# Optimization experiments

Measured on AMD Instinct MI355X. Metric: run time of the kernel, lower is better.

Reference implementation:

```python
import jax, jax.numpy as jnp
import numpy as np

B, IN, H = 4096, 1024, 1024


def setup_inputs() -> dict:
    key = jax.random.key(0)
    ks = jax.random.split(key, 12)
    s = float(np.sqrt(6.0 / (IN + H)))  # xavier-uniform-like scale
    u = lambda k, shp: jax.random.uniform(k, shp, jnp.float32, -s, s)
    return {
        "x": jax.random.normal(ks[0], (B, IN), jnp.float32),
        "h_prev": jax.random.normal(ks[1], (B, H), jnp.float32),
        "c_prev": jax.random.normal(ks[2], (B, H), jnp.float32),
        "n_prev": jnp.ones((B, H), jnp.float32),
        "m_prev": jnp.zeros((B, H), jnp.float32),
        "Wi_x": u(ks[3], (H, IN)), "bi": jnp.zeros((H,), jnp.float32), "Wi_h": u(ks[4], (H, H)),
        "Wf_x": u(ks[5], (H, IN)), "bf": jnp.full((H,), 2.0, jnp.float32), "Wf_h": u(ks[6], (H, H)),
        "Wz_x": u(ks[7], (H, IN)), "bz": jnp.zeros((H,), jnp.float32), "Wz_h": u(ks[8], (H, H)),
        "Wo_x": u(ks[9], (H, IN)), "bo": jnp.zeros((H,), jnp.float32), "Wo_h": u(ks[10], (H, H)),
    }


def reference(x, h_prev, c_prev, n_prev, m_prev,
              Wi_x, bi, Wi_h, Wf_x, bf, Wf_h,
              Wz_x, bz, Wz_h, Wo_x, bo, Wo_h):
    # 8 projections (x-side with bias, h-side without), torch Linear: y = x @ W.T + b
    i_tilde = x @ Wi_x.T + bi + h_prev @ Wi_h.T
    f_aff   = x @ Wf_x.T + bf + h_prev @ Wf_h.T
    z_aff   = x @ Wz_x.T + bz + h_prev @ Wz_h.T
    o_aff   = x @ Wo_x.T + bo + h_prev @ Wo_h.T

    # forget_as_exp=False path: sigmoid forget gate, log-domain stabilizer
    log_f = jnp.log(jnp.clip(jax.nn.sigmoid(f_aff), 1e-8, None))
    m_t = jnp.maximum(log_f + m_prev, i_tilde)
    i_prime = jnp.exp(i_tilde - m_t)
    f_prime = jnp.exp(log_f + m_prev - m_t)

    z = jnp.tanh(z_aff)
    c_t = f_prime * c_prev + i_prime * z
    n_t = f_prime * n_prev + i_prime
    h_t = jax.nn.sigmoid(o_aff) * (c_t / jnp.clip(n_t, 1e-6, None))
    return h_t, c_t, n_t, m_t
```

## Files before the change

kernel.cpp:

```cpp
#include <hip/hip_runtime.h>
#include <stdint.h>


#define B_DIM 4096
#define K_DIM 2048

typedef __bf16 bf16x8 __attribute__((ext_vector_type(8)));
typedef float f32x4 __attribute__((ext_vector_type(4)));
typedef unsigned short ushort8 __attribute__((ext_vector_type(8)));

__device__ __forceinline__ unsigned short f2bf(float f) {
  unsigned u = __float_as_uint(f);
  u += 0x7fffu + ((u >> 16) & 1u);
  return (unsigned short)(u >> 16);
}
__device__ __forceinline__ float bf2f(unsigned short u) {
  return __uint_as_float(((unsigned)u) << 16);
}

__device__ __forceinline__ ushort8 load8_as_bf16(const void* base, size_t off, bool isbf) {
  if (isbf) return *(const ushort8*)((const unsigned short*)base + off);
  const float* f = (const float*)base + off;
  float4 v0 = ((const float4*)f)[0];
  float4 v1 = ((const float4*)f)[1];
  ushort8 o;
  o[0] = f2bf(v0.x); o[1] = f2bf(v0.y); o[2] = f2bf(v0.z); o[3] = f2bf(v0.w);
  o[4] = f2bf(v1.x); o[5] = f2bf(v1.y); o[6] = f2bf(v1.z); o[7] = f2bf(v1.w);
  return o;
}

__global__ void pack_all(const void* __restrict__ xv, const void* __restrict__ hv,
                         const void* __restrict__ Wix, const void* __restrict__ Wih,
                         const void* __restrict__ Wfx, const void* __restrict__ Wfh,
                         const void* __restrict__ Wzx, const void* __restrict__ Wzh,
                         const void* __restrict__ Wox, const void* __restrict__ Woh,
                         unsigned short* __restrict__ Apk, unsigned short* __restrict__ Bpk) {
  const int blk = blockIdx.x;
  const int lane = threadIdx.x & 63;
  const bool isA = blk < 4096;
  const unsigned* disc = (const unsigned*)(isA ? xv : Wix);
  int v = 0;
  if (lane < 32) {
    unsigned e = (disc[lane] >> 7) & 0xFFu;
    v = (e > (isA ? 129u : 122u)) ? 1 : 0;
  }
  const bool isbf = (__ballot(v) == 0ull);

  const int t = (isA ? blk : blk - 4096) * 256 + threadIdx.x;
  const int cl = t & 63;
  const int kt = (t >> 6) & 63;
  const int x16 = t >> 12;
  const int lr = cl & 15;
  const int k = kt * 32 + (cl >> 4) * 8;

  if (isA) {
    int m = x16 * 16 + lr;
    const void* src = (k < 1024) ? xv : hv;
    size_t off = (size_t)m * 1024 + (k & 1023);
    *(ushort8*)(Apk + (size_t)t * 8) = load8_as_bf16(src, off, isbf);
  } else {
    int g = x16 & 3;
    int n = (x16 >> 2) * 16 + lr;
    const void* W;
    if (k < 1024) W = (g == 0) ? Wix : (g == 1) ? Wfx : (g == 2) ? Wzx : Wox;
    else          W = (g == 0) ? Wih : (g == 1) ? Wfh : (g == 2) ? Wzh : Woh;
    size_t off = (size_t)n * 1024 + (k & 1023);
    *(ushort8*)(Bpk + (size_t)t * 8) = load8_as_bf16(W, off, isbf);
  }
}

__global__ __launch_bounds__(256) void gemm_fused(
    const unsigned short* __restrict__ Apk,
    const unsigned short* __restrict__ Bpk,
    const void* __restrict__ bi, const void* __restrict__ bfg,
    const void* __restrict__ bz, const void* __restrict__ bo,
    const void* __restrict__ c_prev, const void* __restrict__ n_prev,
    const void* __restrict__ m_prev,
    float* __restrict__ out)
{
  const int tid  = threadIdx.x;
  const int wave = tid >> 6;
  const int lane = tid & 63;
  const int qrow = lane >> 4;
  const int col  = lane & 15;

  const int bx  = blockIdx.x;
  const int mb  = bx & 31;
  const int qb2 = bx >> 5;
  const int wr = wave >> 1, wc = wave & 1;
  const int m64 = mb * 2 + wr;
  const int q   = qb2 * 2 + wc;

  const unsigned short* pa = Apk + (size_t)(m64 * 4) * 32768 + lane * 8;
  const unsigned short* pb = Bpk + (size_t)(q * 4)   * 32768 + lane * 8;

  f32x4 acc[4][4] = {};
  bf16x8 a0[4], b0[4], a1[4], b1[4];

#pragma unroll
  for (int t = 0; t < 4; ++t) {
    a0[t] = *(const bf16x8*)(pa + t * 32768);
    b0[t] = *(const bf16x8*)(pb + t * 32768);
    a1[t] = *(const bf16x8*)(pa + 512 + t * 32768);
    b1[t] = *(const bf16x8*)(pb + 512 + t * 32768);
  }

#define HALF(abuf, bbuf, REFILL, koff)                                         \
  {                                                                            \
    _Pragma("unroll")                                                          \
    for (int ti = 0; ti < 4; ++ti) {                                           \
      _Pragma("unroll")                                                        \
      for (int tj = 0; tj < 4; ++tj)                                           \
        acc[ti][tj] = __builtin_amdgcn_mfma_f32_16x16x32_bf16(                 \
            abuf[ti], bbuf[tj], acc[ti][tj], 0, 0, 0);                         \
      if (REFILL) abuf[ti] = *(const bf16x8*)(pa + (koff) * 512 + ti * 32768); \
    }                                                                          \
    if (REFILL) {                                                              \
      _Pragma("unroll")                                                        \
      for (int t = 0; t < 4; ++t)                                              \
        bbuf[t] = *(const bf16x8*)(pb + (koff) * 512 + t * 32768);             \
    }                                                                          \
  }

  for (int kt = 0; kt < 62; kt += 2) {
    HALF(a0, b0, 1, kt + 2);
    HALF(a1, b1, 1, kt + 3);
  }
  HALF(a0, b0, 0, 0);
  HALF(a1, b1, 0, 0);
#undef HALF

  const bool sbf = (((const unsigned*)n_prev)[0] == 0x3F803F80u);
  const bool bbf = (((const unsigned*)bfg)[0]    == 0x40004000u);
  const int n = q * 16 + col;
  const float bi_n = bbf ? bf2f(((const unsigned short*)bi)[n])  : ((const float*)bi)[n];
  const float bf_n = bbf ? bf2f(((const unsigned short*)bfg)[n]) : ((const float*)bfg)[n];
  const float bz_n = bbf ? bf2f(((const unsigned short*)bz)[n])  : ((const float*)bz)[n];
  const float bo_n = bbf ? bf2f(((const unsigned short*)bo)[n])  : ((const float*)bo)[n];
  const int rowbase = m64 * 64 + qrow * 4;

  float* out_h = out;
  float* out_c = out + 4194304;
  float* out_n = out + 2 * 4194304;
  float* out_m = out + 3 * 4194304;

#pragma unroll
  for (int ti = 0; ti < 4; ++ti) {
#pragma unroll
    for (int r = 0; r < 4; ++r) {
      int row = rowbase + ti * 16 + r;
      int idx = row * 1024 + n;
      float it = acc[ti][0][r] + bi_n;
      float fa = acc[ti][1][r] + bf_n;
      float za = acc[ti][2][r] + bz_n;
      float oa = acc[ti][3][r] + bo_n;
      float cp  = sbf ? bf2f(((const unsigned short*)c_prev)[idx]) : ((const float*)c_prev)[idx];
      float npv = sbf ? bf2f(((const unsigned short*)n_prev)[idx]) : ((const float*)n_prev)[idx];
      float mp  = sbf ? bf2f(((const unsigned short*)m_prev)[idx]) : ((const float*)m_prev)[idx];

      float sf = 1.f / (1.f + __expf(-fa));
      sf = fmaxf(sf, 1e-8f);
      float lf = __logf(sf);
      float mt = fmaxf(lf + mp, it);
      float ip = __expf(it - mt);
      float fp = __expf(lf + mp - mt);
      float zc = fminf(fmaxf(za, -15.f), 15.f);
      float e2 = __expf(2.f * zc);
      float z  = (e2 - 1.f) / (e2 + 1.f);
      float ct = fp * cp + ip * z;
      float nt = fp * npv + ip;
      float so = 1.f / (1.f + __expf(-oa));
      float ht = so * (ct / fmaxf(nt, 1e-6f));

      out_h[idx] = ht;
      out_c[idx] = ct;
      out_n[idx] = nt;
      out_m[idx] = mt;
    }
  }
}

extern "C" void kernel_launch(void* const* d_in, const int* in_sizes, int n_in,
                              void* d_out, int out_size, void* d_ws, size_t ws_size,
                              hipStream_t stream) {
  const void* x      = d_in[0];
  const void* h_prev = d_in[1];
  const void* c_prev = d_in[2];
  const void* n_prev = d_in[3];
  const void* m_prev = d_in[4];
  const void* Wi_x = d_in[5];
  const void* bi   = d_in[6];
  const void* Wi_h = d_in[7];
  const void* Wf_x = d_in[8];
  const void* bf   = d_in[9];
  const void* Wf_h = d_in[10];
  const void* Wz_x = d_in[11];
  const void* bz   = d_in[12];
  const void* Wz_h = d_in[13];
  const void* Wo_x = d_in[14];
  const void* bo   = d_in[15];
  const void* Wo_h = d_in[16];

  unsigned short* Apk = (unsigned short*)d_ws;
  unsigned short* Bpk = Apk + (size_t)B_DIM * K_DIM;

  pack_all<<<8192, 256, 0, stream>>>(x, h_prev, Wi_x, Wi_h, Wf_x, Wf_h,
                                     Wz_x, Wz_h, Wo_x, Wo_h, Apk, Bpk);
  gemm_fused<<<1024, 256, 0, stream>>>(Apk, Bpk, bi, bf, bz, bo,
                                       c_prev, n_prev, m_prev,
                                       (float*)d_out);
}
```

Measured before the change: 280.3 us.

## Rewrite GEMM as 256x256 LDS-tiled, double-buffered kernel with async global-to-LDS loads

The pack kernel now writes plain row-major bf16 A and B (B rows interleaved by gate in groups of 16) instead of MFMA-fragment order. The GEMM moves from register-only per-wave tiles that read straight from global memory to 256x256 block tiles staged in XOR-swizzled shared memory through global_load_lds. Loads are double-buffered across eight interleaved phases with barriers and setprio around the MFMA bursts, and block IDs are swizzled. This is meant to raise data reuse and cut global/L2 traffic, at the cost of more registers (128 accumulators), barrier overhead and only 256 blocks on the device.

```diff
diff --git a/kernel.cpp b/kernel.cpp
--- a/kernel.cpp
+++ b/kernel.cpp
@@ -46,30 +46,77 @@
   }
   const bool isbf = (__ballot(v) == 0ull);
 
-  const int t = (isA ? blk : blk - 4096) * 256 + threadIdx.x;
-  const int cl = t & 63;
-  const int kt = (t >> 6) & 63;
-  const int x16 = t >> 12;
-  const int lr = cl & 15;
-  const int k = kt * 32 + (cl >> 4) * 8;
-
+  const int k = threadIdx.x * 8;
   if (isA) {
-    int m = x16 * 16 + lr;
+    const int m = blk;
     const void* src = (k < 1024) ? xv : hv;
     size_t off = (size_t)m * 1024 + (k & 1023);
-    *(ushort8*)(Apk + (size_t)t * 8) = load8_as_bf16(src, off, isbf);
+    *(ushort8*)(Apk + (size_t)m * 2048 + k) = load8_as_bf16(src, off, isbf);
   } else {
-    int g = x16 & 3;
-    int n = (x16 >> 2) * 16 + lr;
+    const int br = blk - 4096;
+    const int g = (br >> 4) & 3;
+    const int wrow = ((br >> 6) << 4) | (br & 15);
     const void* W;
     if (k < 1024) W = (g == 0) ? Wix : (g == 1) ? Wfx : (g == 2) ? Wzx : Wox;
     else          W = (g == 0) ? Wih : (g == 1) ? Wfh : (g == 2) ? Wzh : Woh;
-    size_t off = (size_t)n * 1024 + (k & 1023);
-    *(ushort8*)(Bpk + (size_t)t * 8) = load8_as_bf16(W, off, isbf);
-  }
-}
-
-__global__ __launch_bounds__(256) void gemm_fused(
+    size_t off = (size_t)wrow * 1024 + (k & 1023);
+    *(ushort8*)(Bpk + (size_t)br * 2048 + k) = load8_as_bf16(W, off, isbf);
+  }
+}
+
+
+__device__ __forceinline__ void gload16(const unsigned short* g, unsigned short* l) {
+  __builtin_amdgcn_global_load_lds(
+      (__attribute__((address_space(1))) void*)g,
+      (__attribute__((address_space(3))) void*)l, 16, 0, 0);
+}
+
+#define SCHED0 __builtin_amdgcn_sched_barrier(0)
+#define BAR    __builtin_amdgcn_s_barrier()
+#define VM4    asm volatile("s_waitcnt vmcnt(4)" ::: "memory")
+#define VM0    asm volatile("s_waitcnt vmcnt(0)" ::: "memory")
+#define NOWAIT ((void)0)
+#define NOSTAGE ((void)0)
+#define LGKM0  { asm volatile("s_waitcnt lgkmcnt(0)" ::: "memory"); SCHED0; }
+
+#define STAGE_HALF(buf, ab, hf, kt) {                                          \
+    _Pragma("unroll")                                                          \
+    for (int r_ = 0; r_ < 2; ++r_) {                                           \
+      const unsigned short* g_ = (ab ? sB : sA) +                              \
+          (size_t)((r_ * 128 + (hf) * (ab ? 32 : 64)) * 2048 + (kt) * 64);     \
+      gload16(g_, &lds[buf][ab][(hf) * 128 + r_ * 64 + w * 8][0]);             \
+    } }
+
+#define RD_A(buf, mh)                                                          \
+  _Pragma("unroll")                                                            \
+  for (int mi = 0; mi < 4; ++mi) {                                             \
+    fA[mi][0] = *(const bf16x8*)(&lds[buf][0][0][0] + ((mh)*128 + mi*16)*64 + aBase + csw0); \
+    fA[mi][1] = *(const bf16x8*)(&lds[buf][0][0][0] + ((mh)*128 + mi*16)*64 + aBase + csw1); \
+  }
+#define RD_B(buf, nh, FB)                                                      \
+  _Pragma("unroll")                                                            \
+  for (int nf = 0; nf < 2; ++nf) {                                             \
+    FB[nf][0] = *(const bf16x8*)(&lds[buf][1][0][0] + ((nh)*128 + nf*16)*64 + bBase + csw0); \
+    FB[nf][1] = *(const bf16x8*)(&lds[buf][1][0][0] + ((nh)*128 + nf*16)*64 + bBase + csw1); \
+  }
+
+#define MFMA_Q(mh, nh, FB) {                                                   \
+    __builtin_amdgcn_s_setprio(1);                                             \
+    _Pragma("unroll")                                                          \
+    for (int mi = 0; mi < 4; ++mi)                                             \
+      _Pragma("unroll")                                                        \
+      for (int nf = 0; nf < 2; ++nf)                                           \
+        _Pragma("unroll")                                                      \
+        for (int ks = 0; ks < 2; ++ks)                                         \
+          acc[(mh)*4 + mi][(nh)*2 + nf] = __builtin_amdgcn_mfma_f32_16x16x32_bf16( \
+              fA[mi][ks], FB[nf][ks], acc[(mh)*4 + mi][(nh)*2 + nf], 0, 0, 0); \
+    __builtin_amdgcn_s_setprio(0);                                             \
+  }
+
+#define PH(READS, STAGE, MF, WAIT) {                                           \
+    READS; STAGE; SCHED0; BAR; LGKM0; MF; WAIT; SCHED0; BAR; SCHED0; }
+
+__global__ __launch_bounds__(512, 2) void gemm_fused(
     const unsigned short* __restrict__ Apk,
     const unsigned short* __restrict__ Bpk,
     const void* __restrict__ bi, const void* __restrict__ bfg,
@@ -78,66 +125,68 @@
     const void* __restrict__ m_prev,
     float* __restrict__ out)
 {
+  __shared__ unsigned short lds[2][2][256][64];
+
   const int tid  = threadIdx.x;
-  const int wave = tid >> 6;
+  const int w    = tid >> 6;
   const int lane = tid & 63;
-  const int qrow = lane >> 4;
-  const int col  = lane & 15;
-
-  const int bx  = blockIdx.x;
-  const int mb  = bx & 31;
-  const int qb2 = bx >> 5;
-  const int wr = wave >> 1, wc = wave & 1;
-  const int m64 = mb * 2 + wr;
-  const int q   = qb2 * 2 + wc;
-
-  const unsigned short* pa = Apk + (size_t)(m64 * 4) * 32768 + lane * 8;
-  const unsigned short* pb = Bpk + (size_t)(q * 4)   * 32768 + lane * 8;
-
-  f32x4 acc[4][4] = {};
-  bf16x8 a0[4], b0[4], a1[4], b1[4];
-
-#pragma unroll
-  for (int t = 0; t < 4; ++t) {
-    a0[t] = *(const bf16x8*)(pa + t * 32768);
-    b0[t] = *(const bf16x8*)(pb + t * 32768);
-    a1[t] = *(const bf16x8*)(pa + 512 + t * 32768);
-    b1[t] = *(const bf16x8*)(pb + 512 + t * 32768);
-  }
-
-#define HALF(abuf, bbuf, REFILL, koff)                                         \
-  {                                                                            \
-    _Pragma("unroll")                                                          \
-    for (int ti = 0; ti < 4; ++ti) {                                           \
-      _Pragma("unroll")                                                        \
-      for (int tj = 0; tj < 4; ++tj)                                           \
-        acc[ti][tj] = __builtin_amdgcn_mfma_f32_16x16x32_bf16(                 \
-            abuf[ti], bbuf[tj], acc[ti][tj], 0, 0, 0);                         \
-      if (REFILL) abuf[ti] = *(const bf16x8*)(pa + (koff) * 512 + ti * 32768); \
-    }                                                                          \
-    if (REFILL) {                                                              \
-      _Pragma("unroll")                                                        \
-      for (int t = 0; t < 4; ++t)                                              \
-        bbuf[t] = *(const bf16x8*)(pb + (koff) * 512 + t * 32768);             \
-    }                                                                          \
-  }
-
-  for (int kt = 0; kt < 62; kt += 2) {
-    HALF(a0, b0, 1, kt + 2);
-    HALF(a1, b1, 1, kt + 3);
-  }
-  HALF(a0, b0, 0, 0);
-  HALF(a1, b1, 0, 0);
-#undef HALF
+  const int wm   = w >> 2;
+  const int wn   = w & 3;
+  const int lcol = lane & 15;
+
+  const int bid = blockIdx.x;
+  const int swz = (bid & 7) * 32 + (bid >> 3);
+  const int bm = swz >> 4;
+  const int bn = swz & 15;
+
+  const int l3 = lane >> 3;
+  const int cg = (lane & 7) ^ l3;
+  const unsigned short* sA = Apk + (size_t)(bm * 256 + w * 8 + l3) * 2048 + cg * 8;
+  const unsigned short* sB = Bpk + (size_t)(bn * 256 + (w >> 2) * 64 + (w & 3) * 8 + l3) * 2048 + cg * 8;
+
+  const int csw0 = (((lane >> 4)    ) ^ (lane & 7)) * 8;
+  const int csw1 = ((4 + (lane >> 4)) ^ (lane & 7)) * 8;
+  const int aBase = (wm * 64 + lcol) * 64;
+  const int bBase = (wn * 32 + lcol) * 64;
+
+  f32x4 acc[8][4] = {};
+  bf16x8 fA[4][2], fB0[2][2], fB1[2][2];
+
+  STAGE_HALF(0, 0, 0, 0); SCHED0;
+  STAGE_HALF(0, 1, 0, 0); SCHED0;
+  STAGE_HALF(0, 0, 1, 0); SCHED0;
+  STAGE_HALF(0, 1, 1, 0); SCHED0;
+  STAGE_HALF(1, 0, 0, 1); SCHED0;
+  STAGE_HALF(1, 1, 0, 1); SCHED0;
+  VM4; SCHED0; BAR; SCHED0;
+
+  for (int t = 0; t < 30; t += 2) {
+    PH({ RD_A(0, 0); RD_B(0, 0, fB0); }, STAGE_HALF(1, 1, 1, t + 1), MFMA_Q(0, 0, fB0), NOWAIT);
+    PH({ RD_B(0, 1, fB1); },             STAGE_HALF(1, 0, 1, t + 1), MFMA_Q(0, 1, fB1), NOWAIT);
+    PH({ RD_A(0, 1); },                  STAGE_HALF(0, 0, 0, t + 2), MFMA_Q(1, 1, fB1), NOWAIT);
+    PH({ },                              STAGE_HALF(0, 1, 0, t + 2), MFMA_Q(1, 0, fB0), VM4);
+    PH({ RD_A(1, 0); RD_B(1, 0, fB0); }, STAGE_HALF(0, 1, 1, t + 2), MFMA_Q(0, 0, fB0), NOWAIT);
+    PH({ RD_B(1, 1, fB1); },             STAGE_HALF(0, 0, 1, t + 2), MFMA_Q(0, 1, fB1), NOWAIT);
+    PH({ RD_A(1, 1); },                  STAGE_HALF(1, 0, 0, t + 3), MFMA_Q(1, 1, fB1), NOWAIT);
+    PH({ },                              STAGE_HALF(1, 1, 0, t + 3), MFMA_Q(1, 0, fB0), VM4);
+  }
+  PH({ RD_A(0, 0); RD_B(0, 0, fB0); }, STAGE_HALF(1, 1, 1, 31), MFMA_Q(0, 0, fB0), NOWAIT);
+  PH({ RD_B(0, 1, fB1); },             STAGE_HALF(1, 0, 1, 31), MFMA_Q(0, 1, fB1), NOWAIT);
+  PH({ RD_A(0, 1); },                  NOSTAGE,                 MFMA_Q(1, 1, fB1), NOWAIT);
+  PH({ },                              NOSTAGE,                 MFMA_Q(1, 0, fB0), VM0);
+  PH({ RD_A(1, 0); RD_B(1, 0, fB0); }, NOSTAGE,                 MFMA_Q(0, 0, fB0), NOWAIT);
+  PH({ RD_B(1, 1, fB1); },             NOSTAGE,                 MFMA_Q(0, 1, fB1), NOWAIT);
+  PH({ RD_A(1, 1); },                  NOSTAGE,                 MFMA_Q(1, 1, fB1), NOWAIT);
+  PH({ },                              NOSTAGE,                 MFMA_Q(1, 0, fB0), NOWAIT);
 
   const bool sbf = (((const unsigned*)n_prev)[0] == 0x3F803F80u);
   const bool bbf = (((const unsigned*)bfg)[0]    == 0x40004000u);
-  const int n = q * 16 + col;
+  const int n = (bn * 4 + wn) * 16 + lcol;
   const float bi_n = bbf ? bf2f(((const unsigned short*)bi)[n])  : ((const float*)bi)[n];
   const float bf_n = bbf ? bf2f(((const unsigned short*)bfg)[n]) : ((const float*)bfg)[n];
   const float bz_n = bbf ? bf2f(((const unsigned short*)bz)[n])  : ((const float*)bz)[n];
   const float bo_n = bbf ? bf2f(((const unsigned short*)bo)[n])  : ((const float*)bo)[n];
-  const int rowbase = m64 * 64 + qrow * 4;
+  const int row0 = bm * 256 + wm * 128 + (lane >> 4) * 4;
 
   float* out_h = out;
   float* out_c = out + 4194304;
@@ -145,15 +194,15 @@
   float* out_m = out + 3 * 4194304;
 
 #pragma unroll
-  for (int ti = 0; ti < 4; ++ti) {
+  for (int mi = 0; mi < 8; ++mi) {
 #pragma unroll
     for (int r = 0; r < 4; ++r) {
-      int row = rowbase + ti * 16 + r;
-      int idx = row * 1024 + n;
-      float it = acc[ti][0][r] + bi_n;
-      float fa = acc[ti][1][r] + bf_n;
-      float za = acc[ti][2][r] + bz_n;
-      float oa = acc[ti][3][r] + bo_n;
+      const int row = row0 + mi * 16 + r;
+      const size_t idx = (size_t)row * 1024 + n;
+      float it = acc[mi][0][r] + bi_n;
+      float fa = acc[mi][1][r] + bf_n;
+      float za = acc[mi][2][r] + bz_n;
+      float oa = acc[mi][3][r] + bo_n;
       float cp  = sbf ? bf2f(((const unsigned short*)c_prev)[idx]) : ((const float*)c_prev)[idx];
       float npv = sbf ? bf2f(((const unsigned short*)n_prev)[idx]) : ((const float*)n_prev)[idx];
       float mp  = sbf ? bf2f(((const unsigned short*)m_prev)[idx]) : ((const float*)m_prev)[idx];
@@ -206,7 +255,7 @@
 
   pack_all<<<8192, 256, 0, stream>>>(x, h_prev, Wi_x, Wi_h, Wf_x, Wf_h,
                                      Wz_x, Wz_h, Wo_x, Wo_h, Apk, Bpk);
-  gemm_fused<<<1024, 256, 0, stream>>>(Apk, Bpk, bi, bf, bz, bo,
-                                       c_prev, n_prev, m_prev,
-                                       (float*)d_out);
-}
+  gemm_fused<<<256, 512, 0, stream>>>(Apk, Bpk, bi, bf, bz, bo,
+                                      c_prev, n_prev, m_prev,
+                                      (float*)d_out);
+}
```

Measured after the change: 253.3 us. 1.11x faster.
